# Kernel tuning notes

Measured on AMD Instinct MI355X. Metric: run time of the kernel, lower is better.

Reference implementation:

```python
import jax, jax.numpy as jnp
import numpy as np

C = 1024
H = 16
HS = C // H
HID = 4096
A_MIX = 0.7
B_MIX = 0.3
EPS = 1e-5


def layernorm(x, w, b):
    mu = jnp.mean(x, axis=-1, keepdims=True)
    var = jnp.mean(jnp.square(x - mu), axis=-1, keepdims=True)
    return (x - mu) * jax.lax.rsqrt(var + EPS) * w + b


def setup_inputs() -> dict:
    key = jax.random.key(0)
    ks = jax.random.split(key, 12)
    B, N = 4, 1024
    s = 1.0 / np.sqrt(C)
    sh = 1.0 / np.sqrt(HID)
    return {
        "x": jax.random.normal(ks[0], (B, N, C), jnp.float32),
        "Query": jax.random.normal(ks[1], (B, H, N, HS), jnp.float32),
        "Key": jax.random.normal(ks[2], (B, H, N, HS), jnp.float32),
        "Value": jax.random.normal(ks[3], (B, H, N, HS), jnp.float32),
        "ln_w": jnp.ones((C,), jnp.float32),
        "ln_b": jnp.zeros((C,), jnp.float32),
        "qk_w": jax.random.normal(ks[4], (2 * C, C), jnp.float32) * s,
        "qk_b": jnp.zeros((2 * C,), jnp.float32),
        "v_w": jax.random.normal(ks[5], (C, C), jnp.float32) * s,
        "v_b": jnp.zeros((C,), jnp.float32),
        "out_w": jax.random.normal(ks[6], (C, C), jnp.float32) * s,
        "out_b": jnp.zeros((C,), jnp.float32),
        "mlp_w1": jax.random.normal(ks[7], (HID, C), jnp.float32) * s,
        "mlp_b1": jnp.zeros((HID,), jnp.float32),
        "mlp_w2": jax.random.normal(ks[8], (C, HID), jnp.float32) * sh,
        "mlp_b2": jnp.zeros((C,), jnp.float32),
    }


def reference(x, Query, Key, Value, ln_w, ln_b, qk_w, qk_b, v_w, v_b,
              out_w, out_b, mlp_w1, mlp_b1, mlp_w2, mlp_b2):
    B, N, _ = x.shape
    x1 = x
    xn = layernorm(x, ln_w, ln_b)
    # qk projection -> view (B,N,H,HS,2), permute -> (2,B,H,N,HS)
    qk = (xn @ qk_w.T + qk_b).reshape(B, N, H, HS, 2)
    Q = jnp.transpose(qk[..., 0], (0, 2, 1, 3))  # (B,H,N,HS)
    K = jnp.transpose(qk[..., 1], (0, 2, 1, 3))
    V = jnp.transpose((xn @ v_w.T + v_b).reshape(B, N, H, HS), (0, 2, 1, 3))
    Query = A_MIX * Q + B_MIX * Query
    Key = A_MIX * K + B_MIX * Key
    Value = B_MIX * Value + A_MIX * V
    attn = jnp.einsum('bhqd,bhkd->bhqk', Query, Key) / np.sqrt(HS)
    attn = jax.nn.softmax(attn, axis=-1)  # dropout = identity in eval
    o = jnp.einsum('bhqk,bhkd->bhqd', attn, Value)
    o = jnp.transpose(o, (0, 2, 1, 3)).reshape(B, N, C)
    o = o @ out_w.T + out_b
    x = x1 + o
    x2 = x
    xn2 = layernorm(x, ln_w, ln_b)  # same layernorm params reused
    h = jax.nn.gelu(xn2 @ mlp_w1.T + mlp_b1, approximate=False)
    m = h @ mlp_w2.T + mlp_b2
    return (m + x2, Query, Key, Value)
```

## Files before the change

### kernel.cpp

```cpp
#include <hip/hip_runtime.h>

using bf16x8 = __attribute__((ext_vector_type(8))) __bf16;
using f32x4  = __attribute__((ext_vector_type(4))) float;

#define AS1(p) (const __attribute__((address_space(1))) void*)(p)
#define AS3(p) (__attribute__((address_space(3))) void*)(p)

__device__ __forceinline__ unsigned short f2bf(float f) {
    unsigned int u = __float_as_uint(f);
    unsigned int r = (u + 0x7FFFu + ((u >> 16) & 1u)) >> 16;
    return (unsigned short)r;
}
__device__ __forceinline__ float bf2f(unsigned short u) {
    return __uint_as_float((unsigned int)u << 16);
}

__global__ __launch_bounds__(256) void cvt_kernel(const float* __restrict__ in,
                                                  unsigned short* __restrict__ out,
                                                  int n) {
    int i = (blockIdx.x * 256 + threadIdx.x) * 4;
    if (i < n) {
        float4 v = *(const float4*)(in + i);
        unsigned short o0 = f2bf(v.x), o1 = f2bf(v.y), o2 = f2bf(v.z), o3 = f2bf(v.w);
        ushort4 o = make_ushort4(o0, o1, o2, o3);
        *(ushort4*)(out + i) = o;
    }
}

__global__ __launch_bounds__(256) void ln_kernel(const float* __restrict__ in,
                                                 const float* __restrict__ w,
                                                 const float* __restrict__ b,
                                                 unsigned short* __restrict__ out) {
    const int row = blockIdx.x;
    const int tid = threadIdx.x;
    const float4 v = *(const float4*)(in + (size_t)row * 1024 + tid * 4);
    float s  = v.x + v.y + v.z + v.w;
    float ss = v.x * v.x + v.y * v.y + v.z * v.z + v.w * v.w;
    #pragma unroll
    for (int m = 1; m < 64; m <<= 1) {
        s  += __shfl_xor(s, m, 64);
        ss += __shfl_xor(ss, m, 64);
    }
    __shared__ float red[8];
    if ((tid & 63) == 0) { red[(tid >> 6) * 2] = s; red[(tid >> 6) * 2 + 1] = ss; }
    __syncthreads();
    s  = red[0] + red[2] + red[4] + red[6];
    ss = red[1] + red[3] + red[5] + red[7];
    const float mu  = s * (1.0f / 1024.0f);
    const float var = ss * (1.0f / 1024.0f) - mu * mu;
    const float rstd = rsqrtf(var + 1e-5f);
    const float4 wv = *(const float4*)(w + tid * 4);
    const float4 bv = *(const float4*)(b + tid * 4);
    ushort4 o;
    o.x = f2bf((v.x - mu) * rstd * wv.x + bv.x);
    o.y = f2bf((v.y - mu) * rstd * wv.y + bv.y);
    o.z = f2bf((v.z - mu) * rstd * wv.z + bv.z);
    o.w = f2bf((v.w - mu) * rstd * wv.w + bv.w);
    *(ushort4*)(out + (size_t)row * 1024 + tid * 4) = o;
}

template <int EPI>
__global__ __launch_bounds__(256, 4)
void gemm_bt(const unsigned short* __restrict__ A,
             const unsigned short* __restrict__ W,
             const float* __restrict__ bias,
             int M, int N, int K,
             const float* __restrict__ e0, const float* __restrict__ e1,
             float* __restrict__ o0, float* __restrict__ o1,
             unsigned short* __restrict__ u0, unsigned short* __restrict__ u1) {
    __shared__ unsigned short As[128 * 64];
    __shared__ unsigned short Bs[128 * 64];
    const int tid  = threadIdx.x;
    const int wave = tid >> 6, lane = tid & 63;
    const int wr = wave >> 1, wc = wave & 1;
    const int q15 = lane & 15, g = lane >> 4;
    const int gm0 = blockIdx.y * 128, gn0 = blockIdx.x * 128;

    f32x4 acc[4][4] = {};

    const int srow = lane >> 3;
    const int selm = (((lane & 7) ^ srow) << 3);
    const int rswz = (q15 & 7) << 4;

    for (int k0 = 0; k0 < K; k0 += 64) {
        #pragma unroll
        for (int i = 0; i < 4; ++i) {
            const int r = wave * 32 + i * 8 + srow;
            __builtin_amdgcn_global_load_lds(AS1(A + (size_t)(gm0 + r) * K + k0 + selm),
                                             AS3((char*)As + wave * 4096 + i * 1024), 16, 0, 0);
            __builtin_amdgcn_global_load_lds(AS1(W + (size_t)(gn0 + r) * K + k0 + selm),
                                             AS3((char*)Bs + wave * 4096 + i * 1024), 16, 0, 0);
        }
        __syncthreads();
        #pragma unroll
        for (int kk = 0; kk < 2; ++kk) {
            bf16x8 af[4], bfr[4];
            #pragma unroll
            for (int m = 0; m < 4; ++m)
                af[m] = *(const bf16x8*)((char*)As + (wr * 64 + m * 16 + q15) * 128 +
                                         (((kk * 64 + g * 16)) ^ rswz));
            #pragma unroll
            for (int n = 0; n < 4; ++n)
                bfr[n] = *(const bf16x8*)((char*)Bs + (wc * 64 + n * 16 + q15) * 128 +
                                          (((kk * 64 + g * 16)) ^ rswz));
            #pragma unroll
            for (int m = 0; m < 4; ++m)
                #pragma unroll
                for (int n = 0; n < 4; ++n)
                    acc[m][n] = __builtin_amdgcn_mfma_f32_16x16x32_bf16(af[m], bfr[n], acc[m][n], 0, 0, 0);
        }
        __syncthreads();
    }

    #pragma unroll
    for (int m = 0; m < 4; ++m)
    #pragma unroll
    for (int n = 0; n < 4; ++n)
    #pragma unroll
    for (int j = 0; j < 4; ++j) {
        const int r = gm0 + wr * 64 + m * 16 + g * 4 + j;
        const int c = gn0 + wc * 64 + n * 16 + q15;
        const float val = acc[m][n][j] + bias[c];
        if constexpr (EPI == 0) {
            const int bb = r >> 10, nn = r & 1023;
            const int h = c >> 7, hs = (c >> 1) & 63, isk = c & 1;
            const size_t idx = (((size_t)(bb * 16 + h)) * 1024 + nn) * 64 + hs;
            if (!isk) { const float mx = 0.7f * val + 0.3f * e0[idx]; o0[idx] = mx; u0[idx] = f2bf(mx); }
            else      { const float mx = 0.7f * val + 0.3f * e1[idx]; o1[idx] = mx; u1[idx] = f2bf(mx); }
        } else if constexpr (EPI == 1) {
            const int bb = r >> 10, nn = r & 1023;
            const int h = c >> 6, hs = c & 63;
            const size_t idx = (((size_t)(bb * 16 + h)) * 1024 + nn) * 64 + hs;
            const float mx = 0.7f * val + 0.3f * e0[idx];
            o0[idx] = mx;
            u0[(((size_t)(bb * 16 + h)) * 64 + hs) * 1024 + nn] = f2bf(mx);
        } else if constexpr (EPI == 2) {
            const size_t idx = (size_t)r * N + c;
            o0[idx] = val + e0[idx];
        } else if constexpr (EPI == 3) {
            const float gg = 0.5f * val * (1.0f + erff(val * 0.70710678118f));
            u0[(size_t)r * N + c] = f2bf(gg);
        } else {
            const size_t idx = (size_t)r * N + c;
            o0[idx] = val + e0[idx];
        }
    }
}

__global__ __launch_bounds__(256, 6)
void attn_kernel(const unsigned short* __restrict__ Qb,
                 const unsigned short* __restrict__ Kb,
                 const unsigned short* __restrict__ Vt,
                 unsigned short* __restrict__ Op,
                 float* __restrict__ Mws,
                 float* __restrict__ Lws) {
    const int bh = blockIdx.y;
    const int z  = blockIdx.z;
    const int tid = threadIdx.x, wave = tid >> 6, lane = tid & 63;
    const int qbase = blockIdx.x * 64 + wave * 16;
    const int q15 = lane & 15, g = lane >> 4;

    const unsigned short* Qh = Qb + (size_t)bh * 1024 * 64;
    const unsigned short* Kh = Kb + (size_t)bh * 1024 * 64;
    const unsigned short* Vh = Vt + (size_t)bh * 64 * 1024;

    __shared__ alignas(128) unsigned short Ks[64 * 64];
    __shared__ alignas(128) unsigned short Vs[64 * 64];
    __shared__ alignas(128) unsigned short Ps[4][1024];
    char* const Pb = (char*)Ps[wave] + q15 * 128;
    const int swz = (q15 & 7) << 4;

    const int srow8 = lane >> 3;
    const int selm  = (((lane & 7) ^ srow8) << 3);

    bf16x8 aq[2];
    aq[0] = *(const bf16x8*)&Qh[(size_t)(qbase + q15) * 64 + 0  + g * 8];
    aq[1] = *(const bf16x8*)&Qh[(size_t)(qbase + q15) * 64 + 32 + g * 8];

    f32x4 o[4] = {};
    float mrow = -1e30f, lrow = 0.f;

    const int t0 = z * 8;
    for (int t = t0; t < t0 + 8; ++t) {
        const int kb = t * 64;
        #pragma unroll
        for (int i = 0; i < 2; ++i) {
            const int r = wave * 16 + i * 8 + srow8;
            __builtin_amdgcn_global_load_lds(AS1(Kh + (size_t)(kb + r) * 64 + selm),
                                             AS3((char*)Ks + wave * 2048 + i * 1024), 16, 0, 0);
            __builtin_amdgcn_global_load_lds(AS1(Vh + (size_t)r * 1024 + kb + selm),
                                             AS3((char*)Vs + wave * 2048 + i * 1024), 16, 0, 0);
        }
        __syncthreads();

        f32x4 s[4] = {};
        #pragma unroll
        for (int kt = 0; kt < 4; ++kt) {
            #pragma unroll
            for (int kk = 0; kk < 2; ++kk) {
                const bf16x8 bk = *(const bf16x8*)((char*)Ks + (kt * 16 + q15) * 128 +
                                                   ((kk * 64 + g * 16) ^ swz));
                s[kt] = __builtin_amdgcn_mfma_f32_16x16x32_bf16(bk, aq[kk], s[kt], 0, 0, 0);
            }
        }
        float pm = -1e30f;
        #pragma unroll
        for (int kt = 0; kt < 4; ++kt) {
            s[kt] *= 0.125f;
            pm = fmaxf(pm, fmaxf(fmaxf(s[kt][0], s[kt][1]), fmaxf(s[kt][2], s[kt][3])));
        }
        pm = fmaxf(pm, __shfl_xor(pm, 16, 64));
        pm = fmaxf(pm, __shfl_xor(pm, 32, 64));
        const float mnew = fmaxf(mrow, pm);
        const float alpha = __expf(mrow - mnew);
        mrow = mnew;

        float rs = 0.f;
        #pragma unroll
        for (int kt = 0; kt < 4; ++kt) {
            const float p0 = __expf(s[kt][0] - mnew);
            const float p1 = __expf(s[kt][1] - mnew);
            const float p2 = __expf(s[kt][2] - mnew);
            const float p3 = __expf(s[kt][3] - mnew);
            rs += (p0 + p1) + (p2 + p3);
            uint2 pk;
            pk.x = (unsigned int)f2bf(p0) | ((unsigned int)f2bf(p1) << 16);
            pk.y = (unsigned int)f2bf(p2) | ((unsigned int)f2bf(p3) << 16);
            *(uint2*)(Pb + (((kt * 32 + g * 8) ^ swz))) = pk;
        }
        rs += __shfl_xor(rs, 16, 64);
        rs += __shfl_xor(rs, 32, 64);
        lrow = lrow * alpha + rs;

        float af[4];
        #pragma unroll
        for (int j = 0; j < 4; ++j) af[j] = __shfl(alpha, g * 4 + j, 64);
        #pragma unroll
        for (int dt = 0; dt < 4; ++dt)
            #pragma unroll
            for (int j = 0; j < 4; ++j) o[dt][j] *= af[j];

        #pragma unroll
        for (int Bb = 0; Bb < 2; ++Bb) {
            const bf16x8 pa = *(const bf16x8*)(Pb + (((Bb * 64 + g * 16) ^ swz)));
            #pragma unroll
            for (int dt = 0; dt < 4; ++dt) {
                const bf16x8 vb = *(const bf16x8*)((char*)Vs + (dt * 16 + q15) * 128 +
                                                   ((Bb * 64 + g * 16) ^ swz));
                o[dt] = __builtin_amdgcn_mfma_f32_16x16x32_bf16(pa, vb, o[dt], 0, 0, 0);
            }
        }
        __syncthreads();
    }

    #pragma unroll
    for (int dt = 0; dt < 4; ++dt)
        #pragma unroll
        for (int j = 0; j < 4; ++j) {
            const int q = qbase + g * 4 + j;
            Op[(((size_t)z * 64 + bh) * 1024 + q) * 64 + dt * 16 + q15] = f2bf(o[dt][j]);
        }
    if (g == 0) {
        const size_t mi = ((size_t)z * 64 + bh) * 1024 + qbase + q15;
        Mws[mi] = mrow;
        Lws[mi] = lrow;
    }
}

__global__ __launch_bounds__(256)
void attn_combine(const unsigned short* __restrict__ Op,
                  const float* __restrict__ Mws,
                  const float* __restrict__ Lws,
                  unsigned short* __restrict__ Ob) {
    const int e4 = blockIdx.x * 256 + threadIdx.x;
    const int d0 = (e4 & 15) * 4;
    const int q  = (e4 >> 4) & 1023;
    const int bh = e4 >> 14;
    const size_t base0 = (((size_t)bh) * 1024 + q) * 64 + d0;
    const size_t base1 = (((size_t)(64 + bh)) * 1024 + q) * 64 + d0;
    const ushort4 a = *(const ushort4*)&Op[base0];
    const ushort4 c = *(const ushort4*)&Op[base1];
    const size_t mi0 = (size_t)bh * 1024 + q;
    const size_t mi1 = mi0 + 64 * 1024;
    const float m0 = Mws[mi0], m1 = Mws[mi1];
    const float l0 = Lws[mi0], l1 = Lws[mi1];
    const float m  = fmaxf(m0, m1);
    const float w0 = __expf(m0 - m), w1 = __expf(m1 - m);
    const float inv = 1.0f / (l0 * w0 + l1 * w1);
    ushort4 r;
    r.x = f2bf((bf2f(a.x) * w0 + bf2f(c.x) * w1) * inv);
    r.y = f2bf((bf2f(a.y) * w0 + bf2f(c.y) * w1) * inv);
    r.z = f2bf((bf2f(a.z) * w0 + bf2f(c.z) * w1) * inv);
    r.w = f2bf((bf2f(a.w) * w0 + bf2f(c.w) * w1) * inv);
    const int b = bh >> 4, h = bh & 15;
    *(ushort4*)&Ob[((size_t)(b * 1024 + q)) * 1024 + h * 64 + d0] = r;
}

extern "C" void kernel_launch(void* const* d_in, const int* in_sizes, int n_in,
                              void* d_out, int out_size, void* d_ws, size_t ws_size,
                              hipStream_t stream) {
    (void)in_sizes; (void)n_in; (void)out_size; (void)ws_size;
    const float* x     = (const float*)d_in[0];
    const float* Qin   = (const float*)d_in[1];
    const float* Kin   = (const float*)d_in[2];
    const float* Vin   = (const float*)d_in[3];
    const float* ln_w  = (const float*)d_in[4];
    const float* ln_b  = (const float*)d_in[5];
    const float* qk_w  = (const float*)d_in[6];
    const float* qk_b  = (const float*)d_in[7];
    const float* v_w   = (const float*)d_in[8];
    const float* v_b   = (const float*)d_in[9];
    const float* out_w = (const float*)d_in[10];
    const float* out_b = (const float*)d_in[11];
    const float* w1    = (const float*)d_in[12];
    const float* b1    = (const float*)d_in[13];
    const float* w2    = (const float*)d_in[14];
    const float* b2    = (const float*)d_in[15];

    const size_t FOUR_M = (size_t)4 * 1024 * 1024;
    float* out0 = (float*)d_out;
    float* Qout = out0 + FOUR_M;
    float* Kout = Qout + FOUR_M;
    float* Vout = Kout + FOUR_M;

    char* ws = (char*)d_ws;
    const size_t MB = 1024 * 1024;
    unsigned short* xn   = (unsigned short*)(ws + 0);
    unsigned short* qkwb = (unsigned short*)(ws + 8 * MB);
    unsigned short* vwb  = (unsigned short*)(ws + 12 * MB);
    unsigned short* owb  = (unsigned short*)(ws + 14 * MB);
    unsigned short* w1b  = (unsigned short*)(ws + 16 * MB);
    unsigned short* w2b  = (unsigned short*)(ws + 24 * MB);
    unsigned short* Qbuf = (unsigned short*)(ws + 32 * MB);
    unsigned short* Kbuf = (unsigned short*)(ws + 40 * MB);
    unsigned short* Vtb  = (unsigned short*)(ws + 48 * MB);
    unsigned short* atto = (unsigned short*)(ws + 56 * MB);
    unsigned short* hbuf = (unsigned short*)(ws + 32 * MB);
    float* y1 = (float*)(ws + 64 * MB);
    unsigned short* Oprt = (unsigned short*)(ws + 64 * MB);
    float* Mws = (float*)(ws + 8 * MB);
    float* Lws = (float*)(ws + 8 * MB + 512 * 1024);

    cvt_kernel<<<2048, 256, 0, stream>>>(qk_w, qkwb, 2048 * 1024);
    cvt_kernel<<<1024, 256, 0, stream>>>(v_w,  vwb,  1024 * 1024);
    cvt_kernel<<<1024, 256, 0, stream>>>(out_w, owb, 1024 * 1024);
    cvt_kernel<<<4096, 256, 0, stream>>>(w1, w1b, 4096 * 1024);
    cvt_kernel<<<4096, 256, 0, stream>>>(w2, w2b, 4096 * 1024);

    ln_kernel<<<4096, 256, 0, stream>>>(x, ln_w, ln_b, xn);

    {
        dim3 g(2048 / 128, 4096 / 128);
        gemm_bt<0><<<g, 256, 0, stream>>>(xn, qkwb, qk_b, 4096, 2048, 1024,
                                          Qin, Kin, Qout, Kout, Qbuf, Kbuf);
    }
    {
        dim3 g(1024 / 128, 4096 / 128);
        gemm_bt<1><<<g, 256, 0, stream>>>(xn, vwb, v_b, 4096, 1024, 1024,
                                          Vin, nullptr, Vout, nullptr, Vtb, nullptr);
    }
    {
        dim3 g(16, 64, 2);
        attn_kernel<<<g, 256, 0, stream>>>(Qbuf, Kbuf, Vtb, Oprt, Mws, Lws);
        attn_combine<<<4096, 256, 0, stream>>>(Oprt, Mws, Lws, atto);
    }
    {
        dim3 g(1024 / 128, 4096 / 128);
        gemm_bt<2><<<g, 256, 0, stream>>>(atto, owb, out_b, 4096, 1024, 1024,
                                          x, nullptr, y1, nullptr, nullptr, nullptr);
    }
    ln_kernel<<<4096, 256, 0, stream>>>(y1, ln_w, ln_b, xn);
    {
        dim3 g(4096 / 128, 4096 / 128);
        gemm_bt<3><<<g, 256, 0, stream>>>(xn, w1b, b1, 4096, 4096, 1024,
                                          nullptr, nullptr, nullptr, nullptr, hbuf, nullptr);
    }
    {
        dim3 g(1024 / 128, 4096 / 128);
        gemm_bt<4><<<g, 256, 0, stream>>>(hbuf, w2b, b2, 4096, 1024, 4096,
                                          y1, nullptr, out0, nullptr, nullptr, nullptr);
    }
}
```

Baseline: 292.8 us.

## Double-buffer GEMM K-loop, remap workgroups to XCDs, fuse QK and V projections

The GEMM now uses two 32-wide K stages in LDS. The next tile's global-to-LDS load is issued before computing on the current one, which cuts from two barriers per K step to one. Workgroup indices are permuted across the 8 chiplets (XCDs) for better L2 locality. The QK and V projections are merged into a single 3072-column GEMM with a split epilogue. This saves one launch and fills the device better, at the cost of a new swizzle pattern and a per-element branch in the epilogue.

```diff
diff --git a/kernel.cpp b/kernel.cpp
--- a/kernel.cpp
+++ b/kernel.cpp
@@ -21,8 +21,7 @@
     int i = (blockIdx.x * 256 + threadIdx.x) * 4;
     if (i < n) {
         float4 v = *(const float4*)(in + i);
-        unsigned short o0 = f2bf(v.x), o1 = f2bf(v.y), o2 = f2bf(v.z), o3 = f2bf(v.w);
-        ushort4 o = make_ushort4(o0, o1, o2, o3);
+        ushort4 o = make_ushort4(f2bf(v.x), f2bf(v.y), f2bf(v.z), f2bf(v.w));
         *(ushort4*)(out + i) = o;
     }
 }
@@ -64,53 +63,82 @@
 void gemm_bt(const unsigned short* __restrict__ A,
              const unsigned short* __restrict__ W,
              const float* __restrict__ bias,
+             const float* __restrict__ bias2,
              int M, int N, int K,
              const float* __restrict__ e0, const float* __restrict__ e1,
+             const float* __restrict__ e2,
              float* __restrict__ o0, float* __restrict__ o1,
-             unsigned short* __restrict__ u0, unsigned short* __restrict__ u1) {
-    __shared__ unsigned short As[128 * 64];
-    __shared__ unsigned short Bs[128 * 64];
+             float* __restrict__ o2,
+             unsigned short* __restrict__ u0, unsigned short* __restrict__ u1,
+             unsigned short* __restrict__ u2) {
+    __shared__ unsigned short As[2][128 * 32];
+    __shared__ unsigned short Bs[2][128 * 32];
     const int tid  = threadIdx.x;
     const int wave = tid >> 6, lane = tid & 63;
     const int wr = wave >> 1, wc = wave & 1;
     const int q15 = lane & 15, g = lane >> 4;
-    const int gm0 = blockIdx.y * 128, gn0 = blockIdx.x * 128;
+
+    const int gx = gridDim.x;
+    const int nwg = gx * gridDim.y;
+    int flat = blockIdx.y * gx + blockIdx.x;
+    flat = (flat & 7) * (nwg >> 3) + (flat >> 3);
+    const int gm0 = (flat / gx) * 128, gn0 = (flat % gx) * 128;
 
     f32x4 acc[4][4] = {};
 
-    const int srow = lane >> 3;
-    const int selm = (((lane & 7) ^ srow) << 3);
-    const int rswz = (q15 & 7) << 4;
-
-    for (int k0 = 0; k0 < K; k0 += 64) {
-        #pragma unroll
-        for (int i = 0; i < 4; ++i) {
-            const int r = wave * 32 + i * 8 + srow;
-            __builtin_amdgcn_global_load_lds(AS1(A + (size_t)(gm0 + r) * K + k0 + selm),
-                                             AS3((char*)As + wave * 4096 + i * 1024), 16, 0, 0);
-            __builtin_amdgcn_global_load_lds(AS1(W + (size_t)(gn0 + r) * K + k0 + selm),
-                                             AS3((char*)Bs + wave * 4096 + i * 1024), 16, 0, 0);
-        }
+    const int srow16 = lane >> 2;
+    const int sslot  = (((lane & 3) ^ ((lane >> 2) & 3) ^ ((lane >> 4) & 3))) << 3;
+    const int rx     = ((q15 ^ (q15 >> 2)) & 3) << 4;
+
+    const unsigned short* Arow = A + (size_t)(gm0 + wave * 32 + srow16) * K + sslot;
+    const unsigned short* Wrow = W + (size_t)(gn0 + wave * 32 + srow16) * K + sslot;
+    const size_t rstep = (size_t)16 * K;
+
+    #define STAGE(kt, buf)                                                              \
+        {                                                                               \
+            const int k0_ = (kt) * 32;                                                  \
+            __builtin_amdgcn_global_load_lds(AS1(Arow + k0_),                           \
+                AS3((char*)As[buf] + wave * 2048), 16, 0, 0);                           \
+            __builtin_amdgcn_global_load_lds(AS1(Arow + rstep + k0_),                   \
+                AS3((char*)As[buf] + wave * 2048 + 1024), 16, 0, 0);                    \
+            __builtin_amdgcn_global_load_lds(AS1(Wrow + k0_),                           \
+                AS3((char*)Bs[buf] + wave * 2048), 16, 0, 0);                           \
+            __builtin_amdgcn_global_load_lds(AS1(Wrow + rstep + k0_),                   \
+                AS3((char*)Bs[buf] + wave * 2048 + 1024), 16, 0, 0);                    \
+        }
+
+    #define COMPUTE(buf)                                                                \
+        {                                                                               \
+            bf16x8 af[4], bfr[4];                                                       \
+            _Pragma("unroll")                                                           \
+            for (int m = 0; m < 4; ++m)                                                 \
+                af[m] = *(const bf16x8*)((char*)As[buf] +                               \
+                         (wr * 64 + m * 16 + q15) * 64 + ((g << 4) ^ rx));              \
+            _Pragma("unroll")                                                           \
+            for (int n = 0; n < 4; ++n)                                                 \
+                bfr[n] = *(const bf16x8*)((char*)Bs[buf] +                              \
+                         (wc * 64 + n * 16 + q15) * 64 + ((g << 4) ^ rx));              \
+            _Pragma("unroll")                                                           \
+            for (int m = 0; m < 4; ++m)                                                 \
+                _Pragma("unroll")                                                       \
+                for (int n = 0; n < 4; ++n)                                             \
+                    acc[m][n] = __builtin_amdgcn_mfma_f32_16x16x32_bf16(                \
+                        af[m], bfr[n], acc[m][n], 0, 0, 0);                             \
+        }
+
+    const int nt = K >> 5;
+    STAGE(0, 0);
+    __syncthreads();
+    #pragma unroll 2
+    for (int t = 0; t < nt - 1; ++t) {
+        const int cur = t & 1;
+        STAGE(t + 1, cur ^ 1);
+        COMPUTE(cur);
         __syncthreads();
-        #pragma unroll
-        for (int kk = 0; kk < 2; ++kk) {
-            bf16x8 af[4], bfr[4];
-            #pragma unroll
-            for (int m = 0; m < 4; ++m)
-                af[m] = *(const bf16x8*)((char*)As + (wr * 64 + m * 16 + q15) * 128 +
-                                         (((kk * 64 + g * 16)) ^ rswz));
-            #pragma unroll
-            for (int n = 0; n < 4; ++n)
-                bfr[n] = *(const bf16x8*)((char*)Bs + (wc * 64 + n * 16 + q15) * 128 +
-                                          (((kk * 64 + g * 16)) ^ rswz));
-            #pragma unroll
-            for (int m = 0; m < 4; ++m)
-                #pragma unroll
-                for (int n = 0; n < 4; ++n)
-                    acc[m][n] = __builtin_amdgcn_mfma_f32_16x16x32_bf16(af[m], bfr[n], acc[m][n], 0, 0, 0);
-        }
-        __syncthreads();
-    }
+    }
+    COMPUTE((nt - 1) & 1);
+    #undef STAGE
+    #undef COMPUTE
 
     #pragma unroll
     for (int m = 0; m < 4; ++m)
@@ -120,27 +148,33 @@
     for (int j = 0; j < 4; ++j) {
         const int r = gm0 + wr * 64 + m * 16 + g * 4 + j;
         const int c = gn0 + wc * 64 + n * 16 + q15;
-        const float val = acc[m][n][j] + bias[c];
         if constexpr (EPI == 0) {
             const int bb = r >> 10, nn = r & 1023;
-            const int h = c >> 7, hs = (c >> 1) & 63, isk = c & 1;
-            const size_t idx = (((size_t)(bb * 16 + h)) * 1024 + nn) * 64 + hs;
-            if (!isk) { const float mx = 0.7f * val + 0.3f * e0[idx]; o0[idx] = mx; u0[idx] = f2bf(mx); }
-            else      { const float mx = 0.7f * val + 0.3f * e1[idx]; o1[idx] = mx; u1[idx] = f2bf(mx); }
-        } else if constexpr (EPI == 1) {
-            const int bb = r >> 10, nn = r & 1023;
-            const int h = c >> 6, hs = c & 63;
-            const size_t idx = (((size_t)(bb * 16 + h)) * 1024 + nn) * 64 + hs;
-            const float mx = 0.7f * val + 0.3f * e0[idx];
-            o0[idx] = mx;
-            u0[(((size_t)(bb * 16 + h)) * 64 + hs) * 1024 + nn] = f2bf(mx);
+            if (c < 2048) {
+                const float val = acc[m][n][j] + bias[c];
+                const int h = c >> 7, hs = (c >> 1) & 63, isk = c & 1;
+                const size_t idx = (((size_t)(bb * 16 + h)) * 1024 + nn) * 64 + hs;
+                if (!isk) { const float mx = 0.7f * val + 0.3f * e0[idx]; o0[idx] = mx; u0[idx] = f2bf(mx); }
+                else      { const float mx = 0.7f * val + 0.3f * e1[idx]; o1[idx] = mx; u1[idx] = f2bf(mx); }
+            } else {
+                const int cv = c - 2048;
+                const float val = acc[m][n][j] + bias2[cv];
+                const int h = cv >> 6, hs = cv & 63;
+                const size_t idx = (((size_t)(bb * 16 + h)) * 1024 + nn) * 64 + hs;
+                const float mx = 0.7f * val + 0.3f * e2[idx];
+                o2[idx] = mx;
+                u2[(((size_t)(bb * 16 + h)) * 64 + hs) * 1024 + nn] = f2bf(mx);
+            }
         } else if constexpr (EPI == 2) {
+            const float val = acc[m][n][j] + bias[c];
             const size_t idx = (size_t)r * N + c;
             o0[idx] = val + e0[idx];
         } else if constexpr (EPI == 3) {
+            const float val = acc[m][n][j] + bias[c];
             const float gg = 0.5f * val * (1.0f + erff(val * 0.70710678118f));
             u0[(size_t)r * N + c] = f2bf(gg);
         } else {
+            const float val = acc[m][n][j] + bias[c];
             const size_t idx = (size_t)r * N + c;
             o0[idx] = val + e0[idx];
         }
@@ -325,24 +359,23 @@
 
     char* ws = (char*)d_ws;
     const size_t MB = 1024 * 1024;
-    unsigned short* xn   = (unsigned short*)(ws + 0);
-    unsigned short* qkwb = (unsigned short*)(ws + 8 * MB);
-    unsigned short* vwb  = (unsigned short*)(ws + 12 * MB);
-    unsigned short* owb  = (unsigned short*)(ws + 14 * MB);
-    unsigned short* w1b  = (unsigned short*)(ws + 16 * MB);
-    unsigned short* w2b  = (unsigned short*)(ws + 24 * MB);
-    unsigned short* Qbuf = (unsigned short*)(ws + 32 * MB);
-    unsigned short* Kbuf = (unsigned short*)(ws + 40 * MB);
-    unsigned short* Vtb  = (unsigned short*)(ws + 48 * MB);
-    unsigned short* atto = (unsigned short*)(ws + 56 * MB);
-    unsigned short* hbuf = (unsigned short*)(ws + 32 * MB);
+    unsigned short* xn    = (unsigned short*)(ws + 0);
+    unsigned short* qkvwb = (unsigned short*)(ws + 8 * MB);
+    unsigned short* owb   = (unsigned short*)(ws + 14 * MB);
+    unsigned short* w1b   = (unsigned short*)(ws + 16 * MB);
+    unsigned short* w2b   = (unsigned short*)(ws + 24 * MB);
+    unsigned short* Qbuf  = (unsigned short*)(ws + 32 * MB);
+    unsigned short* Kbuf  = (unsigned short*)(ws + 40 * MB);
+    unsigned short* Vtb   = (unsigned short*)(ws + 48 * MB);
+    unsigned short* atto  = (unsigned short*)(ws + 56 * MB);
+    unsigned short* hbuf  = (unsigned short*)(ws + 32 * MB);
     float* y1 = (float*)(ws + 64 * MB);
     unsigned short* Oprt = (unsigned short*)(ws + 64 * MB);
     float* Mws = (float*)(ws + 8 * MB);
     float* Lws = (float*)(ws + 8 * MB + 512 * 1024);
 
-    cvt_kernel<<<2048, 256, 0, stream>>>(qk_w, qkwb, 2048 * 1024);
-    cvt_kernel<<<1024, 256, 0, stream>>>(v_w,  vwb,  1024 * 1024);
+    cvt_kernel<<<2048, 256, 0, stream>>>(qk_w, qkvwb, 2048 * 1024);
+    cvt_kernel<<<1024, 256, 0, stream>>>(v_w,  qkvwb + 2048 * 1024, 1024 * 1024);
     cvt_kernel<<<1024, 256, 0, stream>>>(out_w, owb, 1024 * 1024);
     cvt_kernel<<<4096, 256, 0, stream>>>(w1, w1b, 4096 * 1024);
     cvt_kernel<<<4096, 256, 0, stream>>>(w2, w2b, 4096 * 1024);
@@ -350,14 +383,10 @@
     ln_kernel<<<4096, 256, 0, stream>>>(x, ln_w, ln_b, xn);
 
     {
-        dim3 g(2048 / 128, 4096 / 128);
-        gemm_bt<0><<<g, 256, 0, stream>>>(xn, qkwb, qk_b, 4096, 2048, 1024,
-                                          Qin, Kin, Qout, Kout, Qbuf, Kbuf);
-    }
-    {
-        dim3 g(1024 / 128, 4096 / 128);
-        gemm_bt<1><<<g, 256, 0, stream>>>(xn, vwb, v_b, 4096, 1024, 1024,
-                                          Vin, nullptr, Vout, nullptr, Vtb, nullptr);
+        dim3 g(3072 / 128, 4096 / 128);
+        gemm_bt<0><<<g, 256, 0, stream>>>(xn, qkvwb, qk_b, v_b, 4096, 3072, 1024,
+                                          Qin, Kin, Vin, Qout, Kout, Vout,
+                                          Qbuf, Kbuf, Vtb);
     }
     {
         dim3 g(16, 64, 2);
@@ -366,18 +395,21 @@
     }
     {
         dim3 g(1024 / 128, 4096 / 128);
-        gemm_bt<2><<<g, 256, 0, stream>>>(atto, owb, out_b, 4096, 1024, 1024,
-                                          x, nullptr, y1, nullptr, nullptr, nullptr);
+        gemm_bt<2><<<g, 256, 0, stream>>>(atto, owb, out_b, nullptr, 4096, 1024, 1024,
+                                          x, nullptr, nullptr, y1, nullptr, nullptr,
+                                          nullptr, nullptr, nullptr);
     }
     ln_kernel<<<4096, 256, 0, stream>>>(y1, ln_w, ln_b, xn);
     {
         dim3 g(4096 / 128, 4096 / 128);
-        gemm_bt<3><<<g, 256, 0, stream>>>(xn, w1b, b1, 4096, 4096, 1024,
-                                          nullptr, nullptr, nullptr, nullptr, hbuf, nullptr);
+        gemm_bt<3><<<g, 256, 0, stream>>>(xn, w1b, b1, nullptr, 4096, 4096, 1024,
+                                          nullptr, nullptr, nullptr, nullptr, nullptr, nullptr,
+                                          hbuf, nullptr, nullptr);
     }
     {
         dim3 g(1024 / 128, 4096 / 128);
-        gemm_bt<4><<<g, 256, 0, stream>>>(hbuf, w2b, b2, 4096, 1024, 4096,
-                                          y1, nullptr, out0, nullptr, nullptr, nullptr);
-    }
-}
+        gemm_bt<4><<<g, 256, 0, stream>>>(hbuf, w2b, b2, nullptr, 4096, 1024, 4096,
+                                          y1, nullptr, nullptr, out0, nullptr, nullptr,
+                                          nullptr, nullptr, nullptr);
+    }
+}
```

New measurement: 355.6 us. 1.21x slower.

## Double-buffer GEMM LDS tiles with BK=32 to overlap loads and MFMA

Applied to the files above, without the earlier changes.

Replaces the single 128x64 LDS tile per operand with two ping-pong 128x32 buffers. The next k-slice is issued via global_load_lds while the current one feeds MFMAs, so there is one barrier per k-step instead of two. The swizzle is redone for the 64-byte row layout. Total LDS stays the same, but k-steps are half as deep, which doubles the number of barriers relative to compute.

```diff
diff --git a/kernel.cpp b/kernel.cpp
--- a/kernel.cpp
+++ b/kernel.cpp
@@ -21,8 +21,7 @@
     int i = (blockIdx.x * 256 + threadIdx.x) * 4;
     if (i < n) {
         float4 v = *(const float4*)(in + i);
-        unsigned short o0 = f2bf(v.x), o1 = f2bf(v.y), o2 = f2bf(v.z), o3 = f2bf(v.w);
-        ushort4 o = make_ushort4(o0, o1, o2, o3);
+        ushort4 o = make_ushort4(f2bf(v.x), f2bf(v.y), f2bf(v.z), f2bf(v.w));
         *(ushort4*)(out + i) = o;
     }
 }
@@ -68,8 +67,10 @@
              const float* __restrict__ e0, const float* __restrict__ e1,
              float* __restrict__ o0, float* __restrict__ o1,
              unsigned short* __restrict__ u0, unsigned short* __restrict__ u1) {
-    __shared__ unsigned short As[128 * 64];
-    __shared__ unsigned short Bs[128 * 64];
+    __shared__ unsigned short As0[128 * 32];
+    __shared__ unsigned short Bs0[128 * 32];
+    __shared__ unsigned short As1[128 * 32];
+    __shared__ unsigned short Bs1[128 * 32];
     const int tid  = threadIdx.x;
     const int wave = tid >> 6, lane = tid & 63;
     const int wr = wave >> 1, wc = wave & 1;
@@ -78,39 +79,63 @@
 
     f32x4 acc[4][4] = {};
 
-    const int srow = lane >> 3;
-    const int selm = (((lane & 7) ^ srow) << 3);
-    const int rswz = (q15 & 7) << 4;
-
-    for (int k0 = 0; k0 < K; k0 += 64) {
-        #pragma unroll
-        for (int i = 0; i < 4; ++i) {
-            const int r = wave * 32 + i * 8 + srow;
-            __builtin_amdgcn_global_load_lds(AS1(A + (size_t)(gm0 + r) * K + k0 + selm),
-                                             AS3((char*)As + wave * 4096 + i * 1024), 16, 0, 0);
-            __builtin_amdgcn_global_load_lds(AS1(W + (size_t)(gn0 + r) * K + k0 + selm),
-                                             AS3((char*)Bs + wave * 4096 + i * 1024), 16, 0, 0);
-        }
+    const int srow16 = lane >> 2;
+    const int sslot  = (((lane & 3) ^ (srow16 & 3) ^ ((srow16 >> 2) & 3)) << 3);
+    const int rx     = ((q15 ^ (q15 >> 2)) & 3) << 4;
+
+    const unsigned short* Arow = A + (size_t)(gm0 + wave * 32 + srow16) * K + sslot;
+    const unsigned short* Wrow = W + (size_t)(gn0 + wave * 32 + srow16) * K + sslot;
+    const size_t rstep = (size_t)16 * K;
+
+    #define STAGE(kt, Asb, Bsb)                                                         \
+        {                                                                               \
+            const int k0_ = (kt) * 32;                                                  \
+            __builtin_amdgcn_global_load_lds(AS1(Arow + k0_),                           \
+                AS3((char*)Asb + wave * 2048), 16, 0, 0);                               \
+            __builtin_amdgcn_global_load_lds(AS1(Arow + rstep + k0_),                   \
+                AS3((char*)Asb + wave * 2048 + 1024), 16, 0, 0);                        \
+            __builtin_amdgcn_global_load_lds(AS1(Wrow + k0_),                           \
+                AS3((char*)Bsb + wave * 2048), 16, 0, 0);                               \
+            __builtin_amdgcn_global_load_lds(AS1(Wrow + rstep + k0_),                   \
+                AS3((char*)Bsb + wave * 2048 + 1024), 16, 0, 0);                        \
+        }
+
+    #define COMPUTE(Asb, Bsb)                                                           \
+        {                                                                               \
+            bf16x8 af[4], bfr[4];                                                       \
+            _Pragma("unroll")                                                           \
+            for (int m = 0; m < 4; ++m)                                                 \
+                af[m] = *(const bf16x8*)((char*)Asb +                                   \
+                         (wr * 64 + m * 16 + q15) * 64 + ((g << 4) ^ rx));              \
+            _Pragma("unroll")                                                           \
+            for (int n = 0; n < 4; ++n)                                                 \
+                bfr[n] = *(const bf16x8*)((char*)Bsb +                                  \
+                         (wc * 64 + n * 16 + q15) * 64 + ((g << 4) ^ rx));              \
+            _Pragma("unroll")                                                           \
+            for (int m = 0; m < 4; ++m)                                                 \
+                _Pragma("unroll")                                                       \
+                for (int n = 0; n < 4; ++n)                                             \
+                    acc[m][n] = __builtin_amdgcn_mfma_f32_16x16x32_bf16(                \
+                        af[m], bfr[n], acc[m][n], 0, 0, 0);                             \
+        }
+
+    const int nt = K >> 5;
+    STAGE(0, As0, Bs0);
+    __syncthreads();
+    for (int t = 0; t + 2 < nt; t += 2) {
+        STAGE(t + 1, As1, Bs1);
+        COMPUTE(As0, Bs0);
         __syncthreads();
-        #pragma unroll
-        for (int kk = 0; kk < 2; ++kk) {
-            bf16x8 af[4], bfr[4];
-            #pragma unroll
-            for (int m = 0; m < 4; ++m)
-                af[m] = *(const bf16x8*)((char*)As + (wr * 64 + m * 16 + q15) * 128 +
-                                         (((kk * 64 + g * 16)) ^ rswz));
-            #pragma unroll
-            for (int n = 0; n < 4; ++n)
-                bfr[n] = *(const bf16x8*)((char*)Bs + (wc * 64 + n * 16 + q15) * 128 +
-                                          (((kk * 64 + g * 16)) ^ rswz));
-            #pragma unroll
-            for (int m = 0; m < 4; ++m)
-                #pragma unroll
-                for (int n = 0; n < 4; ++n)
-                    acc[m][n] = __builtin_amdgcn_mfma_f32_16x16x32_bf16(af[m], bfr[n], acc[m][n], 0, 0, 0);
-        }
+        STAGE(t + 2, As0, Bs0);
+        COMPUTE(As1, Bs1);
         __syncthreads();
     }
+    STAGE(nt - 1, As1, Bs1);
+    COMPUTE(As0, Bs0);
+    __syncthreads();
+    COMPUTE(As1, Bs1);
+    #undef STAGE
+    #undef COMPUTE
 
     #pragma unroll
     for (int m = 0; m < 4; ++m)
```

Result: slower. 308.6 us (+5.4%).
